# Optimization experiments

Measured on AMD Instinct MI355X. Metric: run time of the kernel, lower is better.

Reference implementation:

```python
import jax, jax.numpy as jnp
import numpy as np

EPS = 1e-5  # BatchNorm eps


def _unfold3x3(x):
    """torch.nn.Unfold(kernel=3, pad=1, stride=1) -> [B, H*W, 9, C] layout.

    Kernel positions are row-major (kh, kw); index 4 is the center, matching
    x_pn[:, :, 4:5, :] in the torch module.
    """
    B, C, H, W = x.shape
    xp = jnp.pad(x, ((0, 0), (0, 0), (1, 1), (1, 1)))
    patches = jnp.stack([xp[:, :, i:i + H, j:j + W]
                         for i in range(3) for j in range(3)], axis=1)  # [B,9,C,H,W]
    return patches.transpose(0, 3, 4, 1, 2).reshape(B, H * W, 9, C)


def setup_inputs() -> dict:
    key = jax.random.key(0)
    ks = jax.random.split(key, 10)
    B, Cin, Cout, H, W = 2, 64, 64, 64, 2048
    Ctot = 4 + Cin  # 4 meta channels + feature channels
    return {
        "x": jax.random.normal(ks[0], (B, Ctot, H, W), jnp.float32),
        "mask": jax.random.randint(ks[1], (B, 1, H, W), 0, 2, jnp.int32),
        # weight_mlp1: Linear(4 -> Cin, bias=False), torch layout [out, in]
        "W1": jax.random.normal(ks[2], (Cin, 4), jnp.float32) * 0.3,
        "bn1_g": jnp.ones((Cin,), jnp.float32),
        "bn1_b": jnp.zeros((Cin,), jnp.float32),
        "bn1_m": jax.random.normal(ks[3], (Cin,), jnp.float32) * 0.1,
        "bn1_v": jax.random.uniform(ks[4], (Cin,), jnp.float32, 0.5, 1.5),
        # weight_mlp2: Linear(Cin -> 1) (attention head)
        "W2": jax.random.normal(ks[5], (1, Cin), jnp.float32) * 0.1,
        "b2": jnp.zeros((1,), jnp.float32),
        # aggregation_mlp: Linear(9*Cin -> Cout, bias=False)
        "Wagg": jax.random.normal(ks[6], (Cout, 9 * Cin), jnp.float32) * 0.04,
        "bn2_g": jnp.ones((Cout,), jnp.float32),
        "bn2_b": jnp.zeros((Cout,), jnp.float32),
        "bn2_m": jax.random.normal(ks[7], (Cout,), jnp.float32) * 0.1,
        "bn2_v": jax.random.uniform(ks[8], (Cout,), jnp.float32, 0.5, 1.5),
    }


def reference(x, mask, W1, bn1_g, bn1_b, bn1_m, bn1_v, W2, b2,
              Wagg, bn2_g, bn2_b, bn2_m, bn2_v):
    B, Ctot, H, W_ = x.shape
    Cin = W1.shape[0]

    xu = _unfold3x3(x)                       # [B, HW, 9, Ctot]
    feats = xu[..., 4:]                      # [B, HW, 9, Cin]
    pn = xu[..., :4]                         # meta coords of 9 neighbors
    d = pn - pn[:, :, 4:5, :]                # relative to center pixel

    # per-neighbor weight MLP (Linear -> BN(eval) -> ReLU -> Linear)
    w = jnp.einsum('bnkm,cm->bnkc', d, W1)   # [B, HW, 9, Cin]
    w = (w - bn1_m) * (bn1_g * jax.lax.rsqrt(bn1_v + EPS)) + bn1_b
    w = jax.nn.relu(w)
    w = jnp.einsum('bnkc,oc->bnko', w, W2) + b2  # [B, HW, 9, 1]

    mu = _unfold3x3(mask.astype(jnp.float32))    # [B, HW, 9, 1]
    w = w * mu                                   # masked logits
    w = jax.nn.softmax(w[..., 0], axis=-1)[..., None]  # attention over 9 neighbors

    out = (w * feats).reshape(B, H * W_, 9 * Cin)
    y = jnp.einsum('bnf,of->bno', out, Wagg)     # [B, HW, Cout]
    y = (y - bn2_m) * (bn2_g * jax.lax.rsqrt(bn2_v + EPS)) + bn2_b
    y = jax.nn.relu(y)
    # Fold(kernel=1) == reshape back to the feature map
    return y.transpose(0, 2, 1).reshape(B, -1, H, W_)
```

## Files before the change

### kernel.cpp

```cpp
#include <hip/hip_runtime.h>

#define H_ 64
#define W_ 2048
#define HWsz (H_*W_)
#define CIN 64
#define CTOT 68
#define COUT 64

#define XH 66
#define XW 2050

typedef float  f32x4  __attribute__((ext_vector_type(4)));
typedef float  f32x16 __attribute__((ext_vector_type(16)));
typedef short  s16x8  __attribute__((ext_vector_type(8)));

__device__ __forceinline__ unsigned short f2bf(float f) {
    unsigned u = __builtin_bit_cast(unsigned, f);
    unsigned r = u + 0x7fffu + ((u >> 16) & 1u);
    return (unsigned short)(r >> 16);
}

__global__ __launch_bounds__(256) void prep_bw(
    const float* __restrict__ Wagg,
    const float* __restrict__ W1, const float* __restrict__ g1,
    const float* __restrict__ b1, const float* __restrict__ m1,
    const float* __restrict__ v1, const float* __restrict__ W2,
    unsigned short* __restrict__ BwS, float* __restrict__ Wfold)
{
    int tid = threadIdx.x;
    if (blockIdx.x == 0) {
        if (tid < 64) {
            float s1 = g1[tid] * rsqrtf(v1[tid] + 1e-5f);
#pragma unroll
            for (int m = 0; m < 4; ++m) Wfold[tid*8 + m] = W1[tid*4 + m] * s1;
            Wfold[tid*8 + 4] = b1[tid] - m1[tid]*s1;
            Wfold[tid*8 + 5] = W2[tid];
            Wfold[tid*8 + 6] = 0.f;
            Wfold[tid*8 + 7] = 0.f;
        }
        __syncthreads();
        if (tid == 0) {
            float s = 0.f;
            for (int c = 0; c < 64; ++c) s += fmaxf(Wfold[c*8 + 4], 0.f) * Wfold[c*8 + 5];
            Wfold[512] = s;
        }
    }
    int idx = blockIdx.x * 256 + tid;
    if (idx < 4608) {
        int lane = idx & 63;
        int rest = idx >> 6;
        int nt = rest & 1;
        int ks = (rest >> 1) & 3;
        int k9 = rest >> 3;
        int o  = nt*32 + (lane & 31);
        int ch = ks*16 + (lane >> 5)*8;
        const float* src = Wagg + (size_t)o*(9*CIN) + k9*64 + ch;
        s16x8 v8;
#pragma unroll
        for (int j = 0; j < 8; ++j) v8[j] = (short)f2bf(src[j]);
        *(s16x8*)(BwS + (size_t)idx*8) = v8;
    }
}

__global__ __launch_bounds__(256) void prep_xpm(
    const float* __restrict__ x, const int* __restrict__ mask,
    unsigned short* __restrict__ xpad,
    float* __restrict__ pospad, float* __restrict__ maskpad)
{
    int wc = blockIdx.x * 256 + threadIdx.x;
    if (wc >= XW) return;
    int hr = blockIdx.y;
    int b  = blockIdx.z;
    bool interior = (hr >= 1) && (hr <= H_) && (wc >= 1) && (wc <= W_);
    const float* srcf = x + ((size_t)b*CTOT + 4)*HWsz + (size_t)(hr-1)*W_ + (wc-1);
    unsigned short* dst0 = xpad + ((((size_t)b*XH + hr)*8)*XW + wc)*8;
#pragma unroll
    for (int g = 0; g < 8; ++g) {
        s16x8 v8 = {0,0,0,0,0,0,0,0};
        if (interior) {
            const float* s = srcf + (size_t)(g*8)*HWsz;
#pragma unroll
            for (int j = 0; j < 8; ++j) v8[j] = (short)f2bf(s[(size_t)j*HWsz]);
        }
        *(s16x8*)(dst0 + (size_t)g*XW*8) = v8;
    }
    const float* srcp = x + (size_t)b*CTOT*HWsz + (size_t)(hr-1)*W_ + (wc-1);
#pragma unroll
    for (int ch = 0; ch < 4; ++ch) {
        float v = interior ? srcp[(size_t)ch*HWsz] : 0.f;
        pospad[(((size_t)b*XH + hr)*4 + ch)*XW + wc] = v;
    }
    float mv = interior ? (float)mask[((size_t)b*H_ + (hr-1))*W_ + (wc-1)] : 0.f;
    maskpad[((size_t)b*XH + hr)*XW + wc] = mv;
}

__global__ __launch_bounds__(256, 2) void fused_k(
    const unsigned short* __restrict__ xpad,
    const float* __restrict__ pospad, const float* __restrict__ maskpad,
    const unsigned short* __restrict__ BwS, const float* __restrict__ Wfold,
    const float* __restrict__ b2p,
    const float* __restrict__ g2, const float* __restrict__ bb2,
    const float* __restrict__ m2, const float* __restrict__ v2,
    float* __restrict__ out)
{
    __shared__ __align__(16) unsigned short fe[3][8][130][8];
    __shared__ __align__(16) float sw[9][128];

    int tid = threadIdx.x;
    int bx = blockIdx.x, by = blockIdx.y;
    int b = by >> 6, h = by & 63;
    int w0 = bx << 7;
    int lane = tid & 63, wv = tid >> 6;

    const unsigned short* xb = xpad + (size_t)b*XH*8*XW*8;

#pragma unroll
    for (int it = 0; it < 12; ++it) {
        int u = it*4 + wv;
        int chunk = u & 1, g = (u >> 1) & 7, r = u >> 4;
        const unsigned short* gsrc =
            xb + ((((size_t)(h + r)*8 + g)*XW) + w0 + 1 + chunk*64 + lane)*8;
        unsigned short* ldst = &fe[r][g][1 + chunk*64][0];
        __builtin_amdgcn_global_load_lds(
            (const __attribute__((address_space(1))) unsigned int*)gsrc,
            (__attribute__((address_space(3))) unsigned int*)ldst, 16, 0, 0);
    }
    s16x8 haloV = {0,0,0,0,0,0,0,0};
    int hg = 0, hr3 = 0, hc2 = 0;
    if (tid < 48) {
        hc2 = tid & 1; hg = (tid >> 1) & 7; hr3 = tid >> 4;
        haloV = *(const s16x8*)(xb + ((((size_t)(h + hr3)*8 + hg)*XW) + w0 + hc2*129)*8);
    }

    int px = tid & 127, kh = tid >> 7;
    int gw = w0 + px;
    float pA[4][3], pB[4], pc[4], mu[4];
    {
        int rowA = h + (kh ? 2 : 0);
#pragma unroll
        for (int ch = 0; ch < 4; ++ch) {
            const float* pr = pospad + (((size_t)b*XH + rowA)*4 + ch)*XW + gw;
            pA[ch][0] = pr[0]; pA[ch][1] = pr[1]; pA[ch][2] = pr[2];
            const float* p1 = pospad + (((size_t)b*XH + h + 1)*4 + ch)*XW + gw;
            pB[ch] = p1[2*kh];
            pc[ch] = p1[1];
        }
        const float* mr0 = maskpad + ((size_t)b*XH + rowA)*XW + gw;
        const float* mr1 = maskpad + ((size_t)b*XH + h + 1)*XW + gw;
        if (kh == 0) {
            mu[0] = mr0[0]; mu[1] = mr0[1]; mu[2] = mr0[2]; mu[3] = mr1[0];
        } else {
            mu[0] = mr1[2]; mu[1] = mr0[0]; mu[2] = mr0[1]; mu[3] = mr0[2];
        }
    }
    float dd[4][4];
#pragma unroll
    for (int m = 0; m < 4; ++m) {
        if (kh == 0) {
            dd[0][m] = pA[m][0] - pc[m]; dd[1][m] = pA[m][1] - pc[m];
            dd[2][m] = pA[m][2] - pc[m]; dd[3][m] = pB[m]    - pc[m];
        } else {
            dd[0][m] = pB[m]    - pc[m]; dd[1][m] = pA[m][0] - pc[m];
            dd[2][m] = pA[m][1] - pc[m]; dd[3][m] = pA[m][2] - pc[m];
        }
    }

    float lg[4] = {0.f, 0.f, 0.f, 0.f};
    const f32x4* Wf4 = (const f32x4*)Wfold;
#pragma unroll 8
    for (int c = 0; c < CIN; ++c) {
        f32x4 wa = Wf4[2*c];
        f32x4 wb = Wf4[2*c + 1];
#pragma unroll
        for (int t = 0; t < 4; ++t) {
            float v = fmaf(dd[t][0], wa[0], fmaf(dd[t][1], wa[1],
                      fmaf(dd[t][2], wa[2], fmaf(dd[t][3], wa[3], wb[0]))));
            lg[t] += fmaxf(v, 0.f) * wb[1];
        }
    }
    float b2v = b2p[0];
#pragma unroll
    for (int t = 0; t < 4; ++t) {
        int k = kh ? (5 + t) : t;
        sw[k][px] = (lg[t] + b2v) * mu[t];
    }
    if (tid < 48) *(s16x8*)&fe[hr3][hg][hc2*129][0] = haloV;
    __syncthreads();

    if (tid < 128) {
        int p2 = tid, g2w = w0 + p2;
        float mu4 = maskpad[((size_t)b*XH + h + 1)*XW + g2w + 1];
        float lgv[9];
#pragma unroll
        for (int k = 0; k < 9; ++k) if (k != 4) lgv[k] = sw[k][p2];
        lgv[4] = (Wfold[512] + b2v) * mu4;
        float mx = -1e30f;
#pragma unroll
        for (int k = 0; k < 9; ++k) mx = fmaxf(mx, lgv[k]);
        float s = 0.f, e[9];
#pragma unroll
        for (int k = 0; k < 9; ++k) { e[k] = __expf(lgv[k] - mx); s += e[k]; }
        float inv = 1.f / s;
#pragma unroll
        for (int k = 0; k < 9; ++k) sw[k][p2] = e[k] * inv;
    }
    __syncthreads();

    int nt = wv & 1, mh = wv >> 1;
    int l31 = lane & 31, l5 = lane >> 5;

    const f32x16 fz16 = {0.f,0.f,0.f,0.f,0.f,0.f,0.f,0.f,0.f,0.f,0.f,0.f,0.f,0.f,0.f,0.f};
    f32x16 fin[2] = {fz16, fz16};

#pragma unroll
    for (int k9 = 0; k9 < 9; ++k9) {
        const int r = k9/3, dw = k9%3 - 1;

        s16x8 bf[4];
#pragma unroll
        for (int ks = 0; ks < 4; ++ks)
            bf[ks] = *(const s16x8*)(BwS + (size_t)((((k9<<2) + ks)*2 + nt) << 9) + lane*8);

#pragma unroll
        for (int half = 0; half < 2; ++half) {
            int j0 = 1 + mh*64 + half*32 + l31 + dw;
            f32x16 tmp = fz16;
#pragma unroll
            for (int ks = 0; ks < 4; ++ks) {
                s16x8 af = *(const s16x8*)&fe[r][ks*2 + l5][j0][0];
                tmp = __builtin_amdgcn_mfma_f32_32x32x16_bf16(af, bf[ks], tmp, 0, 0, 0);
            }
            int wbase = mh*64 + half*32 + 4*l5;
            f32x4 a0 = *(const f32x4*)&sw[k9][wbase];
            f32x4 a1 = *(const f32x4*)&sw[k9][wbase + 8];
            f32x4 a2 = *(const f32x4*)&sw[k9][wbase + 16];
            f32x4 a3 = *(const f32x4*)&sw[k9][wbase + 24];
#pragma unroll
            for (int c = 0; c < 4; ++c) {
                fin[half][c]      += a0[c] * tmp[c];
                fin[half][4 + c]  += a1[c] * tmp[4 + c];
                fin[half][8 + c]  += a2[c] * tmp[8 + c];
                fin[half][12 + c] += a3[c] * tmp[12 + c];
            }
        }
    }

    int o = nt*32 + l31;
    float sc = g2[o] * rsqrtf(v2[o] + 1e-5f);
    float tc = bb2[o] - m2[o]*sc;
#pragma unroll
    for (int half = 0; half < 2; ++half) {
        float* orow = out + (((size_t)b*COUT + o)*H_ + h)*W_ + w0 + mh*64 + half*32 + 4*l5;
#pragma unroll
        for (int v = 0; v < 4; ++v) {
            f32x4 q;
#pragma unroll
            for (int c = 0; c < 4; ++c) q[c] = fmaxf(fmaf(fin[half][4*v + c], sc, tc), 0.f);
            *(f32x4*)(orow + 8*v) = q;
        }
    }
}

extern "C" void kernel_launch(void* const* d_in, const int* in_sizes, int n_in,
                              void* d_out, int out_size, void* d_ws, size_t ws_size,
                              hipStream_t stream)
{
    const float* x    = (const float*)d_in[0];
    const int*   mask = (const int*)d_in[1];
    const float* W1   = (const float*)d_in[2];
    const float* g1   = (const float*)d_in[3];
    const float* b1   = (const float*)d_in[4];
    const float* m1   = (const float*)d_in[5];
    const float* v1   = (const float*)d_in[6];
    const float* W2   = (const float*)d_in[7];
    const float* b2   = (const float*)d_in[8];
    const float* Wagg = (const float*)d_in[9];
    const float* g2   = (const float*)d_in[10];
    const float* bb2  = (const float*)d_in[11];
    const float* m2   = (const float*)d_in[12];
    const float* v2   = (const float*)d_in[13];
    float* outp = (float*)d_out;

    char* ws = (char*)d_ws;
    unsigned short* xpad    = (unsigned short*)(ws + 0);
    float*          pospad  = (float*)(ws + 34636800);
    float*          maskpad = (float*)(ws + 38966400);
    unsigned short* BwS     = (unsigned short*)(ws + 40048800);
    float*          Wfold   = (float*)(ws + 40122528);

    hipLaunchKernelGGL(prep_bw, dim3(18), dim3(256), 0, stream,
                       Wagg, W1, g1, b1, m1, v1, W2, BwS, Wfold);
    hipLaunchKernelGGL(prep_xpm, dim3((XW + 255)/256, XH, 2), dim3(256), 0, stream,
                       x, mask, xpad, pospad, maskpad);
    hipLaunchKernelGGL(fused_k, dim3(W_/128, 128), dim3(256), 0, stream,
                       xpad, pospad, maskpad, BwS, Wfold, b2,
                       g2, bb2, m2, v2, outp);
}
```

Measured before the change: 207.3 us.

## Halve pixel tile per block, swap MFMA operands, and raise occupancy

The fused kernel now handles 64 pixels per block instead of 128, which doubles the grid and shrinks shared memory. Launch bounds go from 2 to 5 blocks per SIMD. The MFMA operands are swapped so weights are the A operand and features the B operand, which makes the attention scale a single scalar per lane and gives output stores coalesced along width. Each wave now computes two neighbour logits instead of four, and the BN2 scale and shift are precomputed into shared memory. The cost is more redundant halo and weight loads per pixel, plus a tighter register budget.

```diff
diff --git a/kernel.cpp b/kernel.cpp
--- a/kernel.cpp
+++ b/kernel.cpp
@@ -94,7 +94,7 @@
     maskpad[((size_t)b*XH + hr)*XW + wc] = mv;
 }
 
-__global__ __launch_bounds__(256, 2) void fused_k(
+__global__ __launch_bounds__(256, 5) void fused_k(
     const unsigned short* __restrict__ xpad,
     const float* __restrict__ pospad, const float* __restrict__ maskpad,
     const unsigned short* __restrict__ BwS, const float* __restrict__ Wfold,
@@ -103,24 +103,24 @@
     const float* __restrict__ m2, const float* __restrict__ v2,
     float* __restrict__ out)
 {
-    __shared__ __align__(16) unsigned short fe[3][8][130][8];
-    __shared__ __align__(16) float sw[9][128];
+    __shared__ __align__(16) unsigned short fe[3][8][66][8];
+    __shared__ __align__(16) float sw[9][64];
+    __shared__ __align__(16) float sbn[2][64];
 
     int tid = threadIdx.x;
     int bx = blockIdx.x, by = blockIdx.y;
     int b = by >> 6, h = by & 63;
-    int w0 = bx << 7;
+    int w0 = bx << 6;
     int lane = tid & 63, wv = tid >> 6;
 
     const unsigned short* xb = xpad + (size_t)b*XH*8*XW*8;
 
 #pragma unroll
-    for (int it = 0; it < 12; ++it) {
+    for (int it = 0; it < 6; ++it) {
         int u = it*4 + wv;
-        int chunk = u & 1, g = (u >> 1) & 7, r = u >> 4;
-        const unsigned short* gsrc =
-            xb + ((((size_t)(h + r)*8 + g)*XW) + w0 + 1 + chunk*64 + lane)*8;
-        unsigned short* ldst = &fe[r][g][1 + chunk*64][0];
+        int g = u & 7, r = u >> 3;
+        const unsigned short* gsrc = xb + ((((size_t)(h + r)*8 + g)*XW) + w0 + 1 + lane)*8;
+        unsigned short* ldst = &fe[r][g][1][0];
         __builtin_amdgcn_global_load_lds(
             (const __attribute__((address_space(1))) unsigned int*)gsrc,
             (__attribute__((address_space(3))) unsigned int*)ldst, 16, 0, 0);
@@ -129,70 +129,61 @@
     int hg = 0, hr3 = 0, hc2 = 0;
     if (tid < 48) {
         hc2 = tid & 1; hg = (tid >> 1) & 7; hr3 = tid >> 4;
-        haloV = *(const s16x8*)(xb + ((((size_t)(h + hr3)*8 + hg)*XW) + w0 + hc2*129)*8);
-    }
-
-    int px = tid & 127, kh = tid >> 7;
+        haloV = *(const s16x8*)(xb + ((((size_t)(h + hr3)*8 + hg)*XW) + w0 + hc2*65)*8);
+    }
+    if (tid >= 192) {
+        int o = tid - 192;
+        float sc = g2[o] * rsqrtf(v2[o] + 1e-5f);
+        sbn[0][o] = sc;
+        sbn[1][o] = bb2[o] - m2[o]*sc;
+    }
+
+    int px = tid & 63, grp = wv;
+    int k0 = 2*grp + (grp >> 1);
+    int k1 = k0 + 1;
+    const float* pb = pospad + (size_t)b*XH*4*XW;
+    const float* mb = maskpad + (size_t)b*XH*XW;
     int gw = w0 + px;
-    float pA[4][3], pB[4], pc[4], mu[4];
+
+    float pc[4], dd[2][4], mu[2];
+#pragma unroll
+    for (int ch = 0; ch < 4; ++ch)
+        pc[ch] = pb[((size_t)(h+1)*4 + ch)*XW + gw + 1];
     {
-        int rowA = h + (kh ? 2 : 0);
+        int r0 = k0/3, d0 = k0%3, r1 = k1/3, d1 = k1%3;
 #pragma unroll
         for (int ch = 0; ch < 4; ++ch) {
-            const float* pr = pospad + (((size_t)b*XH + rowA)*4 + ch)*XW + gw;
-            pA[ch][0] = pr[0]; pA[ch][1] = pr[1]; pA[ch][2] = pr[2];
-            const float* p1 = pospad + (((size_t)b*XH + h + 1)*4 + ch)*XW + gw;
-            pB[ch] = p1[2*kh];
-            pc[ch] = p1[1];
-        }
-        const float* mr0 = maskpad + ((size_t)b*XH + rowA)*XW + gw;
-        const float* mr1 = maskpad + ((size_t)b*XH + h + 1)*XW + gw;
-        if (kh == 0) {
-            mu[0] = mr0[0]; mu[1] = mr0[1]; mu[2] = mr0[2]; mu[3] = mr1[0];
-        } else {
-            mu[0] = mr1[2]; mu[1] = mr0[0]; mu[2] = mr0[1]; mu[3] = mr0[2];
-        }
-    }
-    float dd[4][4];
-#pragma unroll
-    for (int m = 0; m < 4; ++m) {
-        if (kh == 0) {
-            dd[0][m] = pA[m][0] - pc[m]; dd[1][m] = pA[m][1] - pc[m];
-            dd[2][m] = pA[m][2] - pc[m]; dd[3][m] = pB[m]    - pc[m];
-        } else {
-            dd[0][m] = pB[m]    - pc[m]; dd[1][m] = pA[m][0] - pc[m];
-            dd[2][m] = pA[m][1] - pc[m]; dd[3][m] = pA[m][2] - pc[m];
-        }
-    }
-
-    float lg[4] = {0.f, 0.f, 0.f, 0.f};
+            dd[0][ch] = pb[((size_t)(h+r0)*4 + ch)*XW + gw + d0] - pc[ch];
+            dd[1][ch] = pb[((size_t)(h+r1)*4 + ch)*XW + gw + d1] - pc[ch];
+        }
+        mu[0] = mb[(size_t)(h+r0)*XW + gw + d0];
+        mu[1] = mb[(size_t)(h+r1)*XW + gw + d1];
+    }
+
+    float lg[2] = {0.f, 0.f};
     const f32x4* Wf4 = (const f32x4*)Wfold;
 #pragma unroll 8
     for (int c = 0; c < CIN; ++c) {
         f32x4 wa = Wf4[2*c];
         f32x4 wb = Wf4[2*c + 1];
 #pragma unroll
-        for (int t = 0; t < 4; ++t) {
+        for (int t = 0; t < 2; ++t) {
             float v = fmaf(dd[t][0], wa[0], fmaf(dd[t][1], wa[1],
                       fmaf(dd[t][2], wa[2], fmaf(dd[t][3], wa[3], wb[0]))));
             lg[t] += fmaxf(v, 0.f) * wb[1];
         }
     }
     float b2v = b2p[0];
-#pragma unroll
-    for (int t = 0; t < 4; ++t) {
-        int k = kh ? (5 + t) : t;
-        sw[k][px] = (lg[t] + b2v) * mu[t];
-    }
-    if (tid < 48) *(s16x8*)&fe[hr3][hg][hc2*129][0] = haloV;
+    sw[k0][px] = (lg[0] + b2v) * mu[0];
+    sw[k1][px] = (lg[1] + b2v) * mu[1];
+    if (tid < 48) *(s16x8*)&fe[hr3][hg][hc2*65][0] = haloV;
     __syncthreads();
 
-    if (tid < 128) {
-        int p2 = tid, g2w = w0 + p2;
-        float mu4 = maskpad[((size_t)b*XH + h + 1)*XW + g2w + 1];
+    if (tid < 64) {
+        float mu4 = mb[(size_t)(h+1)*XW + w0 + tid + 1];
         float lgv[9];
 #pragma unroll
-        for (int k = 0; k < 9; ++k) if (k != 4) lgv[k] = sw[k][p2];
+        for (int k = 0; k < 9; ++k) if (k != 4) lgv[k] = sw[k][tid];
         lgv[4] = (Wfold[512] + b2v) * mu4;
         float mx = -1e30f;
 #pragma unroll
@@ -202,7 +193,7 @@
         for (int k = 0; k < 9; ++k) { e[k] = __expf(lgv[k] - mx); s += e[k]; }
         float inv = 1.f / s;
 #pragma unroll
-        for (int k = 0; k < 9; ++k) sw[k][p2] = e[k] * inv;
+        for (int k = 0; k < 9; ++k) sw[k][tid] = e[k] * inv;
     }
     __syncthreads();
 
@@ -210,53 +201,39 @@
     int l31 = lane & 31, l5 = lane >> 5;
 
     const f32x16 fz16 = {0.f,0.f,0.f,0.f,0.f,0.f,0.f,0.f,0.f,0.f,0.f,0.f,0.f,0.f,0.f,0.f};
-    f32x16 fin[2] = {fz16, fz16};
+    f32x16 fin = fz16;
 
 #pragma unroll
     for (int k9 = 0; k9 < 9; ++k9) {
-        const int r = k9/3, dw = k9%3 - 1;
-
-        s16x8 bf[4];
+        const int r = k9/3, dwp = k9%3;
+        int col = mh*32 + l31 + dwp;
+
+        s16x8 aw[4];
 #pragma unroll
         for (int ks = 0; ks < 4; ++ks)
-            bf[ks] = *(const s16x8*)(BwS + (size_t)((((k9<<2) + ks)*2 + nt) << 9) + lane*8);
-
-#pragma unroll
-        for (int half = 0; half < 2; ++half) {
-            int j0 = 1 + mh*64 + half*32 + l31 + dw;
-            f32x16 tmp = fz16;
-#pragma unroll
-            for (int ks = 0; ks < 4; ++ks) {
-                s16x8 af = *(const s16x8*)&fe[r][ks*2 + l5][j0][0];
-                tmp = __builtin_amdgcn_mfma_f32_32x32x16_bf16(af, bf[ks], tmp, 0, 0, 0);
-            }
-            int wbase = mh*64 + half*32 + 4*l5;
-            f32x4 a0 = *(const f32x4*)&sw[k9][wbase];
-            f32x4 a1 = *(const f32x4*)&sw[k9][wbase + 8];
-            f32x4 a2 = *(const f32x4*)&sw[k9][wbase + 16];
-            f32x4 a3 = *(const f32x4*)&sw[k9][wbase + 24];
-#pragma unroll
-            for (int c = 0; c < 4; ++c) {
-                fin[half][c]      += a0[c] * tmp[c];
-                fin[half][4 + c]  += a1[c] * tmp[4 + c];
-                fin[half][8 + c]  += a2[c] * tmp[8 + c];
-                fin[half][12 + c] += a3[c] * tmp[12 + c];
-            }
-        }
-    }
-
-    int o = nt*32 + l31;
-    float sc = g2[o] * rsqrtf(v2[o] + 1e-5f);
-    float tc = bb2[o] - m2[o]*sc;
-#pragma unroll
-    for (int half = 0; half < 2; ++half) {
-        float* orow = out + (((size_t)b*COUT + o)*H_ + h)*W_ + w0 + mh*64 + half*32 + 4*l5;
-#pragma unroll
-        for (int v = 0; v < 4; ++v) {
-            f32x4 q;
-#pragma unroll
-            for (int c = 0; c < 4; ++c) q[c] = fmaxf(fmaf(fin[half][4*v + c], sc, tc), 0.f);
-            *(f32x4*)(orow + 8*v) = q;
+            aw[ks] = *(const s16x8*)(BwS + (size_t)((((k9<<2) + ks)*2 + nt) << 9) + lane*8);
+
+        f32x16 tmp = fz16;
+#pragma unroll
+        for (int ks = 0; ks < 4; ++ks) {
+            s16x8 bfr = *(const s16x8*)&fe[r][ks*2 + l5][col][0];
+            tmp = __builtin_amdgcn_mfma_f32_32x32x16_bf16(aw[ks], bfr, tmp, 0, 0, 0);
+        }
+        float wsc = sw[k9][mh*32 + l31];
+#pragma unroll
+        for (int c = 0; c < 16; ++c) fin[c] += wsc * tmp[c];
+    }
+
+    int obase = nt*32 + 4*l5;
+    float* od = out + (((size_t)b*COUT + obase)*H_ + h)*W_ + w0 + mh*32 + l31;
+#pragma unroll
+    for (int v = 0; v < 4; ++v) {
+        f32x4 sc4 = *(const f32x4*)&sbn[0][obase + 8*v];
+        f32x4 tc4 = *(const f32x4*)&sbn[1][obase + 8*v];
+#pragma unroll
+        for (int c = 0; c < 4; ++c) {
+            float val = fmaxf(fmaf(fin[4*v + c], sc4[c], tc4[c]), 0.f);
+            od[(size_t)(8*v + c)*HWsz] = val;
         }
     }
 }
@@ -292,7 +269,7 @@
                        Wagg, W1, g1, b1, m1, v1, W2, BwS, Wfold);
     hipLaunchKernelGGL(prep_xpm, dim3((XW + 255)/256, XH, 2), dim3(256), 0, stream,
                        x, mask, xpad, pospad, maskpad);
-    hipLaunchKernelGGL(fused_k, dim3(W_/128, 128), dim3(256), 0, stream,
+    hipLaunchKernelGGL(fused_k, dim3(W_/64, 128), dim3(256), 0, stream,
                        xpad, pospad, maskpad, BwS, Wfold, b2,
                        g2, bb2, m2, v2, outp);
 }
```

Result: faster. 202.4 us (-2.3%).
